# Kernel optimization log

Hardware: AMD Instinct MI355X
Metric: run time of the kernel (lower is better)

The kernel has to match this reference:

```python
import jax, jax.numpy as jnp
from jax import lax
import numpy as np

NUM_HEADS = 8
KW = 3  # window kernel size

def _avgpool3(x):
    # x: [B,C,H,W]; AvgPool2d(3,1,1) with count_include_pad=True -> sum/9
    s = lax.reduce_window(x, 0.0, lax.add, (1, 1, KW, KW), (1, 1, 1, 1),
                          ((0, 0), (0, 0), (1, 1), (1, 1)))
    return s / (KW * KW)

def _unfold3(y):
    # y: [B,h,w,C] -> [B,h,w,9,C]; patch index ordered row-major (kh,kw)
    B, h, w, C = y.shape
    yp = jnp.pad(y, ((0, 0), (1, 1), (1, 1), (0, 0)))
    return jnp.stack([yp[:, i:i + h, j:j + w, :]
                      for i in range(KW) for j in range(KW)], axis=3)

def setup_inputs():
    key = jax.random.key(0)
    ks = jax.random.split(key, 9)
    B, C, H, W = 8, 256, 64, 64
    sd = 0.02
    return {
        "x": jax.random.normal(ks[0], (B, C, H, W), jnp.float32),
        "W_qkv": jax.random.normal(ks[1], (4 * C, C), jnp.float32) * sd,
        "b_qkv": jnp.zeros((4 * C,), jnp.float32),
        "W1": jax.random.normal(ks[2], (C // 2, C), jnp.float32) * sd,
        "b1": jnp.zeros((C // 2,), jnp.float32),
        "W2": jax.random.normal(ks[3], (C, C // 2), jnp.float32) * sd,
        "b2": jnp.zeros((C,), jnp.float32),
        "Wp": jax.random.normal(ks[4], (C, C), jnp.float32) * sd,
        "bp": jnp.zeros((C,), jnp.float32),
    }

def reference(x, W_qkv, b_qkv, W1, b1, W2, b2, Wp, bp):
    B, C, H, W = x.shape
    nH = NUM_HEADS
    hd = C // nH
    scale = hd ** -0.5
    # avg pool (stride 1 keeps spatial dims), to channels-last
    y = _avgpool3(x).transpose(0, 2, 3, 1)                 # [B,h,w,C]
    qkv = y @ W_qkv.T + b_qkv                              # [B,h,w,4C]
    qkv = qkv.reshape(B, H, W, C, 4)
    q, k, v, chans = qkv[..., 0], qkv[..., 1], qkv[..., 2], qkv[..., 3]
    # channel gate
    g = jax.nn.sigmoid(jax.nn.relu(chans @ W1.T + b1) @ W2.T + b2)  # [B,h,w,C]
    # local window attention: each query attends to its 3x3 neighborhood
    qh = q.reshape(B, H, W, nH, hd)                        # [B,h,w,n,d]
    kp = _unfold3(k).reshape(B, H, W, KW * KW, nH, hd)     # [B,h,w,9,n,d]
    vp = _unfold3(v).reshape(B, H, W, KW * KW, nH, hd)
    attn = jnp.einsum('bhwnd,bhwknd->bhwnk', qh, kp) * scale
    attn = jax.nn.softmax(attn, axis=-1)
    out = jnp.einsum('bhwnk,bhwknd->bhwnd', attn, vp).reshape(B, H, W, C)
    out = out * g + out
    out = out @ Wp.T + bp
    return out.transpose(0, 3, 1, 2)                       # [B,C,H,W]
```

## Files before the change

kernel.cpp:

```cpp
#include <hip/hip_runtime.h>
#include <stdint.h>

typedef __bf16    bf16x8 __attribute__((ext_vector_type(8)));
typedef float     f32x4  __attribute__((ext_vector_type(4)));
typedef uint32_t  u32x4  __attribute__((ext_vector_type(4)));

#define MFMA(a,b,c) __builtin_amdgcn_mfma_f32_16x16x32_bf16((a),(b),(c),0,0,0)

__device__ __align__(16) uint16_t g_y [8*64*64*256];
__device__ __align__(16) uint16_t g_wpk[393216];

#define WQF 0
#define WKF 65536
#define WVF 131072
#define WCF 196608
#define W1F 262144
#define W2F 294912
#define WPF 327680

static __device__ __forceinline__ float b2f(uint32_t u){ return __builtin_bit_cast(float, u<<16); }
static __device__ __forceinline__ uint32_t f2b(float f){
  uint32_t x = __builtin_bit_cast(uint32_t, f);
  return (x + 0x7fffu + ((x>>16)&1u)) >> 16;
}

__global__ __launch_bounds__(512) void kprep(const float* __restrict__ x,
    const float* __restrict__ Wqkv, const float* __restrict__ W1,
    const float* __restrict__ W2, const float* __restrict__ Wp){
  int t = threadIdx.x;
  int bid = blockIdx.x;
  if (bid < 1024){
    __shared__ __align__(16) uint16_t sm[3*128*82];
    uint32_t* smw = (uint32_t*)sm;
    int b = bid >> 7, h = (bid >> 1) & 63, ch = (bid & 1) << 7;
    for (int i=t; i<384; i+=512){
      int base = i*41;
      smw[base+3]  = 0;
      smw[base+36] = 0;
    }
    if (h==0 || h==63){
      int hh = (h==0) ? 0 : 2;
      for (int i=t; i<5248; i+=512) smw[hh*5248 + i] = 0;
    }
    #pragma unroll
    for (int i=0;i<12;i++){
      int id = t + 512*i;
      int w4 = id&15, c = (id>>4)&127, hh = id>>11;
      int gy = h - 1 + hh;
      if ((unsigned)gy < 64u){
        f32x4 ld = *(const f32x4*)&x[(((b*256+ch+c)*64+gy)*64) + w4*4];
        int wb = (((hh*128+c)*82 + 8 + w4*4) >> 1);
        smw[wb+0] = f2b(ld[0]) | (f2b(ld[1])<<16);
        smw[wb+1] = f2b(ld[2]) | (f2b(ld[3])<<16);
      }
    }
    __syncthreads();
    int c = t & 127, wsel = t >> 7;
    int r0 = c*82, r1 = r0 + 128*82, r2 = r1 + 128*82;
    int w0 = wsel*16;
    float csp = b2f(sm[r0+w0+7]) + b2f(sm[r1+w0+7]) + b2f(sm[r2+w0+7]);
    float csc = b2f(sm[r0+w0+8]) + b2f(sm[r1+w0+8]) + b2f(sm[r2+w0+8]);
    uint16_t* dst = g_y + ((b*64+h)*64)*256 + ch + c;
    for (int j2=0;j2<16;j2++){
      int w = w0 + j2;
      float csn = b2f(sm[r0+w+9]) + b2f(sm[r1+w+9]) + b2f(sm[r2+w+9]);
      float yv = (csp + csc + csn) * (1.0f/9.0f);
      dst[w*256] = (uint16_t)f2b(yv);
      csp = csc; csc = csn;
    }
  } else {
    int idx = (bid - 1024)*512 + t;
    int j = idx & 7, lane = (idx>>3)&63;
    int n16 = lane & 15, q4 = lane>>4;
    float v;
    if (idx < 262144){
      int tt = idx >> 16, l = idx & 65535;
      int s = (l>>9)&7, nt = l>>12;
      v = Wqkv[(4*(nt*16+n16) + tt)*256 + s*32 + q4*8 + j];
    } else if (idx < 294912){
      int l = idx - 262144;
      int s = (l>>9)&7, nt = l>>12;
      v = W1[(nt*16+n16)*256 + s*32 + q4*8 + j];
    } else if (idx < 327680){
      int l = idx - 294912;
      int s = (l>>9)&3, nt = l>>11;
      v = W2[(nt*16+n16)*128 + s*32 + q4*8 + j];
    } else {
      int l = idx - 327680;
      int s = (l>>9)&7, nt = l>>12;
      v = Wp[(nt*16+n16)*256 + s*32 + q4*8 + j];
    }
    g_wpk[idx] = (uint16_t)f2b(v);
  }
}

#define YSTR  264
#define HSTR  136
#define K2_QS 15840
#define K2_KS 20192
#define K2_VS 28352
#define MCH   0
#define MHS   8448
#define MAO   15840
#define MAOSTR 266
__global__ __launch_bounds__(512,4) void kattn(const float* __restrict__ bqkv,
    const float* __restrict__ b1, const float* __restrict__ b2v,
    const float* __restrict__ bp, float* __restrict__ out){
  __shared__ __align__(16) uint16_t sm[36512];
  int t = threadIdx.x;
  int lane = t & 63, wave = t >> 6;
  int n16 = lane & 15, quad = lane >> 4;
  int bid = blockIdx.x;
  int bb = bid >> 7, ty = (bid >> 3) & 15, tx = bid & 7;

  uint32_t opk[2][8];
  uint32_t chp[16];

  #pragma unroll
  for (int i=0;i<4;i++){
    int id = t + 512*i;
    if (id < 1920){
      int hp = id >> 5, c8 = id & 31;
      int py = hp/10, px = hp - py*10;
      int gy = ty*4 + py - 1, gx = tx*8 + px - 1;
      u32x4 ld = {0,0,0,0};
      if ((unsigned)gy<64u && (unsigned)gx<64u)
        ld = *(const u32x4*)&g_y[((bb*64+gy)*64+gx)*256 + c8*8];
      *(u32x4*)&sm[hp*YSTR + c8*8] = ld;
    }
  }
  __syncthreads();

  #pragma unroll
  for (int hf=0; hf<2; hf++){
    {
      int ntg = hf*8 + wave;
      bf16x8 Bq[8];
      #pragma unroll
      for (int s=0;s<8;s++) Bq[s] = *(const bf16x8*)&g_wpk[WQF + ((ntg*8+s)*64+lane)*8];
      float bq = bqkv[4*(ntg*16+n16) + 0];
      int colB = wave*16;
      #pragma unroll
      for (int mt=0; mt<2; mt++){
        f32x4 a = {0.f,0.f,0.f,0.f};
        int m = mt*16 + n16;
        int hrow = 10*(m>>3) + (m&7) + 11;
        #pragma unroll
        for (int s=0;s<8;s++){
          bf16x8 A = *(const bf16x8*)&sm[hrow*YSTR + s*32 + quad*8];
          a = MFMA(A, Bq[s], a);
        }
        #pragma unroll
        for (int r=0;r<4;r++){
          int row = mt*16 + quad*4 + r;
          sm[K2_QS + row*HSTR + colB + n16] = (uint16_t)f2b(a[r] + bq);
        }
      }
    }
    __syncthreads();
    {
      int ntg = hf*8 + wave;
      bf16x8 Bk[8], Bv[8];
      #pragma unroll
      for (int s=0;s<8;s++){
        Bk[s] = *(const bf16x8*)&g_wpk[WKF + ((ntg*8+s)*64+lane)*8];
        Bv[s] = *(const bf16x8*)&g_wpk[WVF + ((ntg*8+s)*64+lane)*8];
      }
      float bk = bqkv[4*(ntg*16+n16) + 1];
      float bv = bqkv[4*(ntg*16+n16) + 2];
      int colB = wave*16;
      #pragma unroll
      for (int mt=0; mt<4; mt++){
        f32x4 ak = {0.f,0.f,0.f,0.f}, av = {0.f,0.f,0.f,0.f};
        int m = mt*16 + n16;
        int mr = (m < 60) ? m : 59;
        #pragma unroll
        for (int s=0;s<8;s++){
          bf16x8 A = *(const bf16x8*)&sm[mr*YSTR + s*32 + quad*8];
          ak = MFMA(A, Bk[s], ak);
          av = MFMA(A, Bv[s], av);
        }
        #pragma unroll
        for (int r=0;r<4;r++){
          int row = mt*16 + quad*4 + r;
          if (row < 60){
            int py = row/10, px = row - py*10;
            int gy = ty*4 + py - 1, gx = tx*8 + px - 1;
            bool ok = ((unsigned)gy<64u) && ((unsigned)gx<64u);
            float vk = ok ? ak[r] + bk : 0.f;
            float vv = ok ? av[r] + bv : 0.f;
            sm[K2_KS + row*HSTR + colB + n16] = (uint16_t)f2b(vk);
            sm[K2_VS + row*HSTR + colB + n16] = (uint16_t)f2b(vv);
          }
        }
      }
    }
    __syncthreads();
    if (wave < 4){
      int p = lane & 31, half = lane >> 5;
      int cb = wave*32 + half*16;
      const uint16_t* qp = &sm[K2_QS + p*HSTR + cb];
      u32x4 qa = *(const u32x4*)qp;
      u32x4 qb = *(const u32x4*)(qp+8);
      float qv[16];
      #pragma unroll
      for (int i=0;i<4;i++){
        qv[2*i]    = b2f(qa[i]&0xffffu); qv[2*i+1]   = b2f(qa[i]>>16);
        qv[8+2*i]  = b2f(qb[i]&0xffffu); qv[8+2*i+1] = b2f(qb[i]>>16);
      }
      int hb = 10*(p>>3) + (p&7) + 11;
      const int off[9] = {-11,-10,-9,-1,0,1,9,10,11};
      float sc[9];
      #pragma unroll
      for (int nb=0;nb<9;nb++){
        const uint16_t* kp = &sm[K2_KS + (hb+off[nb])*HSTR + cb];
        u32x4 ka = *(const u32x4*)kp;
        u32x4 kb = *(const u32x4*)(kp+8);
        float s = 0.f;
        #pragma unroll
        for (int i=0;i<4;i++){
          s += qv[2*i]*b2f(ka[i]&0xffffu)   + qv[2*i+1]*b2f(ka[i]>>16);
          s += qv[8+2*i]*b2f(kb[i]&0xffffu) + qv[8+2*i+1]*b2f(kb[i]>>16);
        }
        s += __shfl_xor(s, 32);
        sc[nb] = s * 0.17677669529663687f;
      }
      float mx = sc[0];
      #pragma unroll
      for (int nb=1;nb<9;nb++) mx = fmaxf(mx, sc[nb]);
      float l = 0.f;
      #pragma unroll
      for (int nb=0;nb<9;nb++){ sc[nb] = __expf(sc[nb]-mx); l += sc[nb]; }
      float inv = 1.f / l;
      float o[16];
      #pragma unroll
      for (int i=0;i<16;i++) o[i]=0.f;
      #pragma unroll
      for (int nb=0;nb<9;nb++){
        float wgt = sc[nb]*inv;
        const uint16_t* vp = &sm[K2_VS + (hb+off[nb])*HSTR + cb];
        u32x4 va = *(const u32x4*)vp;
        u32x4 vb = *(const u32x4*)(vp+8);
        #pragma unroll
        for (int i=0;i<4;i++){
          o[2*i]    += wgt*b2f(va[i]&0xffffu); o[2*i+1]   += wgt*b2f(va[i]>>16);
          o[8+2*i]  += wgt*b2f(vb[i]&0xffffu); o[8+2*i+1] += wgt*b2f(vb[i]>>16);
        }
      }
      #pragma unroll
      for (int i=0;i<8;i++) opk[hf][i] = f2b(o[2*i]) | (f2b(o[2*i+1])<<16);
    } else if (hf == 0){
      #pragma unroll
      for (int jj=0;jj<4;jj++){
        int ntg = (wave-4)*4 + jj;
        bf16x8 Bc[8];
        #pragma unroll
        for (int s=0;s<8;s++) Bc[s] = *(const bf16x8*)&g_wpk[WCF + ((ntg*8+s)*64+lane)*8];
        float bc = bqkv[4*(ntg*16+n16) + 3];
        #pragma unroll
        for (int mt=0; mt<2; mt++){
          f32x4 a = {0.f,0.f,0.f,0.f};
          int m = mt*16 + n16;
          int hrow = 10*(m>>3) + (m&7) + 11;
          #pragma unroll
          for (int s=0;s<8;s++){
            bf16x8 A = *(const bf16x8*)&sm[hrow*YSTR + s*32 + quad*8];
            a = MFMA(A, Bc[s], a);
          }
          chp[(jj*2+mt)*2+0] = f2b(a[0]+bc) | (f2b(a[1]+bc)<<16);
          chp[(jj*2+mt)*2+1] = f2b(a[2]+bc) | (f2b(a[3]+bc)<<16);
        }
      }
    } else {
      #pragma unroll
      for (int jj=0;jj<4;jj++){
        int ntg = (wave-4)*4 + jj;
        int col = ntg*16 + n16;
        #pragma unroll
        for (int mt=0;mt<2;mt++){
          #pragma unroll
          for (int r2=0;r2<2;r2++){
            uint32_t v = chp[(jj*2+mt)*2+r2];
            int row = mt*16 + quad*4 + r2*2;
            sm[MCH + row*264 + col]     = (uint16_t)(v & 0xffffu);
            sm[MCH + (row+1)*264 + col] = (uint16_t)(v >> 16);
          }
        }
      }
    }
    __syncthreads();
  }
  if (wave < 4){
    int p = lane & 31, half = lane >> 5;
    int cb = wave*32 + half*16;
    #pragma unroll
    for (int hf=0;hf<2;hf++)
      #pragma unroll
      for (int i=0;i<8;i++)
        *(uint32_t*)&sm[MAO + p*MAOSTR + hf*128 + cb + 2*i] = opk[hf][i];
  }
  {
    int ntg = wave;
    bf16x8 Bf[8];
    #pragma unroll
    for (int s=0;s<8;s++) Bf[s] = *(const bf16x8*)&g_wpk[W1F + ((ntg*8+s)*64+lane)*8];
    float bs = b1[ntg*16+n16];
    int colB = wave*16;
    #pragma unroll
    for (int mt=0;mt<2;mt++){
      f32x4 a = {0.f,0.f,0.f,0.f};
      #pragma unroll
      for (int s=0;s<8;s++){
        bf16x8 A = *(const bf16x8*)&sm[MCH + (mt*16+n16)*264 + s*32 + quad*8];
        a = MFMA(A, Bf[s], a);
      }
      #pragma unroll
      for (int r=0;r<4;r++){
        int row = mt*16 + quad*4 + r;
        sm[MHS + row*HSTR + colB + n16] = (uint16_t)f2b(fmaxf(a[r]+bs, 0.f));
      }
    }
  }
  __syncthreads();
  #pragma unroll
  for (int jj=0;jj<2;jj++){
    int ntg = wave*2 + jj;
    bf16x8 Bf[4];
    #pragma unroll
    for (int s=0;s<4;s++) Bf[s] = *(const bf16x8*)&g_wpk[W2F + ((ntg*4+s)*64+lane)*8];
    float bs = b2v[ntg*16+n16];
    int colB = ntg*16;
    #pragma unroll
    for (int mt=0;mt<2;mt++){
      f32x4 a = {0.f,0.f,0.f,0.f};
      #pragma unroll
      for (int s=0;s<4;s++){
        bf16x8 A = *(const bf16x8*)&sm[MHS + (mt*16+n16)*HSTR + s*32 + quad*8];
        a = MFMA(A, Bf[s], a);
      }
      #pragma unroll
      for (int r=0;r<4;r++){
        int row = mt*16 + quad*4 + r;
        float gg = 1.f/(1.f+__expf(-(a[r] + bs)));
        float ao = b2f((uint32_t)sm[MAO + row*MAOSTR + colB + n16]);
        sm[MCH + row*264 + colB + n16] = (uint16_t)f2b(ao*(1.f+gg));
      }
    }
  }
  __syncthreads();
  #pragma unroll
  for (int jj=0;jj<2;jj++){
    int ntg = wave*2 + jj;
    bf16x8 Bf[8];
    #pragma unroll
    for (int s=0;s<8;s++) Bf[s] = *(const bf16x8*)&g_wpk[WPF + ((ntg*8+s)*64+lane)*8];
    float bs = bp[ntg*16+n16];
    int colB = ntg*16;
    #pragma unroll
    for (int mt=0;mt<2;mt++){
      f32x4 a = {0.f,0.f,0.f,0.f};
      #pragma unroll
      for (int s=0;s<8;s++){
        bf16x8 A = *(const bf16x8*)&sm[MCH + (mt*16+n16)*264 + s*32 + quad*8];
        a = MFMA(A, Bf[s], a);
      }
      #pragma unroll
      for (int r=0;r<4;r++){
        int row = mt*16 + quad*4 + r;
        sm[MAO + row*MAOSTR + colB + n16] = (uint16_t)f2b(a[r]+bs);
      }
    }
  }
  __syncthreads();
  #pragma unroll
  for (int i=0;i<4;i++){
    int idx = t + 512*i;
    int ix4 = idx&1, iy = (idx>>1)&3, c = idx>>3;
    f32x4 stv;
    #pragma unroll
    for (int j=0;j<4;j++){
      int p = iy*8 + ix4*4 + j;
      stv[j] = b2f((uint32_t)sm[MAO + p*MAOSTR + c]);
    }
    *(f32x4*)&out[(((bb*256+c)*64) + ty*4+iy)*64 + tx*8 + ix4*4] = stv;
  }
}

extern "C" void kernel_launch(void* const* d_in, const int* in_sizes, int n_in,
                              void* d_out, int out_size, void* d_ws, size_t ws_size,
                              hipStream_t stream){
  (void)in_sizes; (void)n_in; (void)d_ws; (void)ws_size; (void)out_size;
  const float* x    = (const float*)d_in[0];
  const float* Wqkv = (const float*)d_in[1];
  const float* bqkv = (const float*)d_in[2];
  const float* W1   = (const float*)d_in[3];
  const float* b1   = (const float*)d_in[4];
  const float* W2   = (const float*)d_in[5];
  const float* b2   = (const float*)d_in[6];
  const float* Wp   = (const float*)d_in[7];
  const float* bp   = (const float*)d_in[8];
  kprep<<<dim3(1792), dim3(512), 0, stream>>>(x, Wqkv, W1, W2, Wp);
  kattn<<<dim3(1024), dim3(512), 0, stream>>>(bqkv, b1, b2, bp, (float*)d_out);
}
```

Measured before the change: 182.0 us.

## Fuse avgpool into attention kernel, computing pooled halo tile from x in LDS

Removes the separate avgpool pass and its bf16 intermediate buffer g_y. The attention kernel now loads a 6x12 raw x halo per tile from NCHW fp32 into LDS, then computes the 3x3 average into the existing 10x10 halo layout. The prep kernel only packs weights. This saves a full write and read of the pooled tensor, but each tile recomputes the pooled halo and reads a larger overlapping input region. LDS use also grows, which may lower occupancy.

Measured after the change: 216.6 us. 1.19x slower.

```diff
diff --git a/kernel.cpp b/kernel.cpp
--- a/kernel.cpp
+++ b/kernel.cpp
@@ -7,7 +7,6 @@
 
 #define MFMA(a,b,c) __builtin_amdgcn_mfma_f32_16x16x32_bf16((a),(b),(c),0,0,0)
 
-__device__ __align__(16) uint16_t g_y [8*64*64*256];
 __device__ __align__(16) uint16_t g_wpk[393216];
 
 #define WQF 0
@@ -24,77 +23,35 @@
   return (x + 0x7fffu + ((x>>16)&1u)) >> 16;
 }
 
-__global__ __launch_bounds__(512) void kprep(const float* __restrict__ x,
-    const float* __restrict__ Wqkv, const float* __restrict__ W1,
-    const float* __restrict__ W2, const float* __restrict__ Wp){
-  int t = threadIdx.x;
-  int bid = blockIdx.x;
-  if (bid < 1024){
-    __shared__ __align__(16) uint16_t sm[3*128*82];
-    uint32_t* smw = (uint32_t*)sm;
-    int b = bid >> 7, h = (bid >> 1) & 63, ch = (bid & 1) << 7;
-    for (int i=t; i<384; i+=512){
-      int base = i*41;
-      smw[base+3]  = 0;
-      smw[base+36] = 0;
-    }
-    if (h==0 || h==63){
-      int hh = (h==0) ? 0 : 2;
-      for (int i=t; i<5248; i+=512) smw[hh*5248 + i] = 0;
-    }
-    #pragma unroll
-    for (int i=0;i<12;i++){
-      int id = t + 512*i;
-      int w4 = id&15, c = (id>>4)&127, hh = id>>11;
-      int gy = h - 1 + hh;
-      if ((unsigned)gy < 64u){
-        f32x4 ld = *(const f32x4*)&x[(((b*256+ch+c)*64+gy)*64) + w4*4];
-        int wb = (((hh*128+c)*82 + 8 + w4*4) >> 1);
-        smw[wb+0] = f2b(ld[0]) | (f2b(ld[1])<<16);
-        smw[wb+1] = f2b(ld[2]) | (f2b(ld[3])<<16);
-      }
-    }
-    __syncthreads();
-    int c = t & 127, wsel = t >> 7;
-    int r0 = c*82, r1 = r0 + 128*82, r2 = r1 + 128*82;
-    int w0 = wsel*16;
-    float csp = b2f(sm[r0+w0+7]) + b2f(sm[r1+w0+7]) + b2f(sm[r2+w0+7]);
-    float csc = b2f(sm[r0+w0+8]) + b2f(sm[r1+w0+8]) + b2f(sm[r2+w0+8]);
-    uint16_t* dst = g_y + ((b*64+h)*64)*256 + ch + c;
-    for (int j2=0;j2<16;j2++){
-      int w = w0 + j2;
-      float csn = b2f(sm[r0+w+9]) + b2f(sm[r1+w+9]) + b2f(sm[r2+w+9]);
-      float yv = (csp + csc + csn) * (1.0f/9.0f);
-      dst[w*256] = (uint16_t)f2b(yv);
-      csp = csc; csc = csn;
-    }
+__global__ __launch_bounds__(256) void kpack(const float* __restrict__ Wqkv,
+    const float* __restrict__ W1, const float* __restrict__ W2,
+    const float* __restrict__ Wp){
+  int idx = blockIdx.x*256 + threadIdx.x;
+  int j = idx & 7, lane = (idx>>3)&63;
+  int n16 = lane & 15, q4 = lane>>4;
+  float v;
+  if (idx < 262144){
+    int t = idx >> 16, l = idx & 65535;
+    int s = (l>>9)&7, nt = l>>12;
+    v = Wqkv[(4*(nt*16+n16) + t)*256 + s*32 + q4*8 + j];
+  } else if (idx < 294912){
+    int l = idx - 262144;
+    int s = (l>>9)&7, nt = l>>12;
+    v = W1[(nt*16+n16)*256 + s*32 + q4*8 + j];
+  } else if (idx < 327680){
+    int l = idx - 294912;
+    int s = (l>>9)&3, nt = l>>11;
+    v = W2[(nt*16+n16)*128 + s*32 + q4*8 + j];
   } else {
-    int idx = (bid - 1024)*512 + t;
-    int j = idx & 7, lane = (idx>>3)&63;
-    int n16 = lane & 15, q4 = lane>>4;
-    float v;
-    if (idx < 262144){
-      int tt = idx >> 16, l = idx & 65535;
-      int s = (l>>9)&7, nt = l>>12;
-      v = Wqkv[(4*(nt*16+n16) + tt)*256 + s*32 + q4*8 + j];
-    } else if (idx < 294912){
-      int l = idx - 262144;
-      int s = (l>>9)&7, nt = l>>12;
-      v = W1[(nt*16+n16)*256 + s*32 + q4*8 + j];
-    } else if (idx < 327680){
-      int l = idx - 294912;
-      int s = (l>>9)&3, nt = l>>11;
-      v = W2[(nt*16+n16)*128 + s*32 + q4*8 + j];
-    } else {
-      int l = idx - 327680;
-      int s = (l>>9)&7, nt = l>>12;
-      v = Wp[(nt*16+n16)*256 + s*32 + q4*8 + j];
-    }
-    g_wpk[idx] = (uint16_t)f2b(v);
-  }
+    int l = idx - 327680;
+    int s = (l>>9)&7, nt = l>>12;
+    v = Wp[(nt*16+n16)*256 + s*32 + q4*8 + j];
+  }
+  g_wpk[idx] = (uint16_t)f2b(v);
 }
 
 #define YSTR  264
+#define XS0   15840
 #define HSTR  136
 #define K2_QS 15840
 #define K2_KS 20192
@@ -103,15 +60,17 @@
 #define MHS   8448
 #define MAO   15840
 #define MAOSTR 266
-__global__ __launch_bounds__(512,4) void kattn(const float* __restrict__ bqkv,
-    const float* __restrict__ b1, const float* __restrict__ b2v,
-    const float* __restrict__ bp, float* __restrict__ out){
-  __shared__ __align__(16) uint16_t sm[36512];
+__global__ __launch_bounds__(512,4) void kattn(const float* __restrict__ x,
+    const float* __restrict__ bqkv, const float* __restrict__ b1,
+    const float* __restrict__ b2v, const float* __restrict__ bp,
+    float* __restrict__ out){
+  __shared__ __align__(16) uint16_t sm[40416];
   int t = threadIdx.x;
   int lane = t & 63, wave = t >> 6;
   int n16 = lane & 15, quad = lane >> 4;
   int bid = blockIdx.x;
   int bb = bid >> 7, ty = (bid >> 3) & 15, tx = bid & 7;
+  int gy0 = ty*4, gx0 = tx*8;
 
   uint32_t opk[2][8];
   uint32_t chp[16];
@@ -119,14 +78,39 @@
   #pragma unroll
   for (int i=0;i<4;i++){
     int id = t + 512*i;
-    if (id < 1920){
-      int hp = id >> 5, c8 = id & 31;
-      int py = hp/10, px = hp - py*10;
-      int gy = ty*4 + py - 1, gx = tx*8 + px - 1;
-      u32x4 ld = {0,0,0,0};
-      if ((unsigned)gy<64u && (unsigned)gx<64u)
-        ld = *(const u32x4*)&g_y[((bb*64+gy)*64+gx)*256 + c8*8];
-      *(u32x4*)&sm[hp*YSTR + c8*8] = ld;
+    int gy = id >> 8, c = id & 255;
+    int Gy = gy0 - 2 + gy;
+    bool rowok = ((unsigned)Gy < 64u);
+    const float* xrow = x + ((bb*256+c)*64 + Gy)*64;
+    float xv[16];
+    #pragma unroll
+    for (int j=0;j<4;j++){
+      int col0 = gx0 - 4 + 4*j;
+      f32x4 ld = {0.f,0.f,0.f,0.f};
+      if (rowok && (unsigned)col0 < 64u)
+        ld = *(const f32x4*)&xrow[col0];
+      xv[4*j+0]=ld[0]; xv[4*j+1]=ld[1]; xv[4*j+2]=ld[2]; xv[4*j+3]=ld[3];
+    }
+    #pragma unroll
+    for (int k=0;k<12;k++)
+      sm[XS0 + (gy*12+k)*256 + c] = (uint16_t)f2b(xv[k+2]);
+  }
+  __syncthreads();
+  #pragma unroll
+  for (int i=0;i<3;i++){
+    int id = t + 512*i;
+    int c = id & 255, py = id >> 8;
+    int xb = XS0 + c;
+    int r0 = (py+0)*12*256, r1 = (py+1)*12*256, r2 = (py+2)*12*256;
+    float s0 = b2f(sm[xb+r0]) + b2f(sm[xb+r1]) + b2f(sm[xb+r2]);
+    float s1 = b2f(sm[xb+r0+256]) + b2f(sm[xb+r1+256]) + b2f(sm[xb+r2+256]);
+    #pragma unroll
+    for (int px=0; px<10; px++){
+      int ko = (px+2)*256;
+      float sn = b2f(sm[xb+r0+ko]) + b2f(sm[xb+r1+ko]) + b2f(sm[xb+r2+ko]);
+      float yv = (s0 + s1 + sn) * (1.0f/9.0f);
+      sm[(py*10+px)*YSTR + c] = (uint16_t)f2b(yv);
+      s0 = s1; s1 = sn;
     }
   }
   __syncthreads();
@@ -399,6 +383,6 @@
   const float* b2   = (const float*)d_in[6];
   const float* Wp   = (const float*)d_in[7];
   const float* bp   = (const float*)d_in[8];
-  kprep<<<dim3(1792), dim3(512), 0, stream>>>(x, Wqkv, W1, W2, Wp);
-  kattn<<<dim3(1024), dim3(512), 0, stream>>>(bqkv, b1, b2, bp, (float*)d_out);
+  kpack<<<dim3(1536), dim3(256), 0, stream>>>(Wqkv, W1, W2, Wp);
+  kattn<<<dim3(1024), dim3(512), 0, stream>>>(x, bqkv, b1, b2, bp, (float*)d_out);
 }
```

## Retile avgpool prep to four rows per block and use native bf16 conversion

Applied to the files above, without the earlier changes.

Each pooling block in the prep kernel now covers 4 output rows by 64 channels instead of 1 row by 128 channels. Six staged input rows serve four output rows, so each x row is read from global memory about half as often, and the prep grid shrinks to match. Float-to-bf16 conversion now uses the compiler's native __bf16 cast instead of manual rounding arithmetic. A __syncthreads between the Q projection and the K/V projection in the attention kernel is also removed to cut barrier cost, which is only safe if those phases never touch overlapping shared memory.

Measured after the change: 176.3 us. 3.2% less time.

```diff
diff --git a/kernel.cpp b/kernel.cpp
--- a/kernel.cpp
+++ b/kernel.cpp
@@ -23,53 +23,63 @@
   uint32_t x = __builtin_bit_cast(uint32_t, f);
   return (x + 0x7fffu + ((x>>16)&1u)) >> 16;
 }
+static __device__ __forceinline__ uint16_t f2bn(float f){
+  return __builtin_bit_cast(uint16_t, (__bf16)f);
+}
+static __device__ __forceinline__ uint32_t pk2(float x, float y){
+  return (uint32_t)f2bn(x) | ((uint32_t)f2bn(y) << 16);
+}
 
 __global__ __launch_bounds__(512) void kprep(const float* __restrict__ x,
     const float* __restrict__ Wqkv, const float* __restrict__ W1,
     const float* __restrict__ W2, const float* __restrict__ Wp){
   int t = threadIdx.x;
   int bid = blockIdx.x;
-  if (bid < 1024){
-    __shared__ __align__(16) uint16_t sm[3*128*82];
+  if (bid < 512){
+    __shared__ __align__(16) uint16_t sm[6*64*82];
     uint32_t* smw = (uint32_t*)sm;
-    int b = bid >> 7, h = (bid >> 1) & 63, ch = (bid & 1) << 7;
+    int b = bid >> 6, rem = bid & 63;
+    int hg = rem >> 2, cg = rem & 3;
+    int h0 = hg*4, ch = cg*64;
     for (int i=t; i<384; i+=512){
       int base = i*41;
       smw[base+3]  = 0;
       smw[base+36] = 0;
     }
-    if (h==0 || h==63){
-      int hh = (h==0) ? 0 : 2;
-      for (int i=t; i<5248; i+=512) smw[hh*5248 + i] = 0;
+    if (hg==0){
+      for (int i=t; i<2624; i+=512) smw[i] = 0;
+    }
+    if (hg==15){
+      for (int i=t; i<2624; i+=512) smw[5*2624 + i] = 0;
     }
     #pragma unroll
     for (int i=0;i<12;i++){
       int id = t + 512*i;
-      int w4 = id&15, c = (id>>4)&127, hh = id>>11;
-      int gy = h - 1 + hh;
+      int w4 = id&15, c = (id>>4)&63, hh = id>>10;
+      int gy = h0 - 1 + hh;
       if ((unsigned)gy < 64u){
         f32x4 ld = *(const f32x4*)&x[(((b*256+ch+c)*64+gy)*64) + w4*4];
-        int wb = (((hh*128+c)*82 + 8 + w4*4) >> 1);
-        smw[wb+0] = f2b(ld[0]) | (f2b(ld[1])<<16);
-        smw[wb+1] = f2b(ld[2]) | (f2b(ld[3])<<16);
+        int wb = (((hh*64+c)*82 + 8 + w4*4) >> 1);
+        smw[wb+0] = pk2(ld[0], ld[1]);
+        smw[wb+1] = pk2(ld[2], ld[3]);
       }
     }
     __syncthreads();
-    int c = t & 127, wsel = t >> 7;
-    int r0 = c*82, r1 = r0 + 128*82, r2 = r1 + 128*82;
-    int w0 = wsel*16;
+    int c = t & 63, wsel = (t >> 6) & 1, py = t >> 7;
+    int r0 = ((py+0)*64+c)*82, r1 = ((py+1)*64+c)*82, r2 = ((py+2)*64+c)*82;
+    int w0 = wsel*32;
     float csp = b2f(sm[r0+w0+7]) + b2f(sm[r1+w0+7]) + b2f(sm[r2+w0+7]);
     float csc = b2f(sm[r0+w0+8]) + b2f(sm[r1+w0+8]) + b2f(sm[r2+w0+8]);
-    uint16_t* dst = g_y + ((b*64+h)*64)*256 + ch + c;
-    for (int j2=0;j2<16;j2++){
+    uint16_t* dst = g_y + ((b*64 + h0 + py)*64)*256 + ch + c;
+    for (int j2=0;j2<32;j2++){
       int w = w0 + j2;
       float csn = b2f(sm[r0+w+9]) + b2f(sm[r1+w+9]) + b2f(sm[r2+w+9]);
       float yv = (csp + csc + csn) * (1.0f/9.0f);
-      dst[w*256] = (uint16_t)f2b(yv);
+      dst[w*256] = f2bn(yv);
       csp = csc; csc = csn;
     }
   } else {
-    int idx = (bid - 1024)*512 + t;
+    int idx = (bid - 512)*512 + t;
     int j = idx & 7, lane = (idx>>3)&63;
     int n16 = lane & 15, q4 = lane>>4;
     float v;
@@ -90,7 +100,7 @@
       int s = (l>>9)&7, nt = l>>12;
       v = Wp[(nt*16+n16)*256 + s*32 + q4*8 + j];
     }
-    g_wpk[idx] = (uint16_t)f2b(v);
+    g_wpk[idx] = f2bn(v);
   }
 }
 
@@ -157,7 +167,6 @@
         }
       }
     }
-    __syncthreads();
     {
       int ntg = hf*8 + wave;
       bf16x8 Bk[8], Bv[8];
@@ -399,6 +408,6 @@
   const float* b2   = (const float*)d_in[6];
   const float* Wp   = (const float*)d_in[7];
   const float* bp   = (const float*)d_in[8];
-  kprep<<<dim3(1792), dim3(512), 0, stream>>>(x, Wqkv, W1, W2, Wp);
+  kprep<<<dim3(1280), dim3(512), 0, stream>>>(x, Wqkv, W1, W2, Wp);
   kattn<<<dim3(1024), dim3(512), 0, stream>>>(bqkv, b1, b2, bp, (float*)d_out);
 }
```
